# Kernel optimization log

Hardware: AMD Instinct MI355X
Metric: run time of the kernel (lower is better)

Reference implementation:

```python
import math
import jax, jax.numpy as jnp
import numpy as np

N_GAUSS = 1_000_000
EPS = 1e-8


def setup_inputs() -> dict:
    key = jax.random.key(0)
    k1, k2, k3 = jax.random.split(key, 3)
    init_extent = 50.0
    means = (jax.random.uniform(k1, (N_GAUSS, 3), dtype=jnp.float32) - 0.5) * 2.0 * init_extent
    log_scales = jnp.full((N_GAUSS, 3), math.log(0.05), dtype=jnp.float32)
    quats = jax.random.normal(k2, (N_GAUSS, 4), dtype=jnp.float32)
    sh_coeffs = jax.random.normal(k3, (N_GAUSS, 16, 3), dtype=jnp.float32) * 0.01
    opa_logit = math.log(0.1 / 0.9)  # inverse_sigmoid(init_opacity=0.1)
    opacity_camera = jnp.full((N_GAUSS, 1), opa_logit, dtype=jnp.float32)
    opacity_lidar = jnp.full((N_GAUSS, 1), opa_logit, dtype=jnp.float32)
    camera_to_world = jnp.eye(4, dtype=jnp.float32)
    lidar_to_world = jnp.eye(4, dtype=jnp.float32)
    intrinsics = jnp.array([[1000.0, 0.0, 800.0], [0.0, 1000.0, 450.0], [0.0, 0.0, 1.0]], dtype=jnp.float32)
    return dict(means=means, log_scales=log_scales, quats=quats, sh_coeffs=sh_coeffs,
                opacity_camera=opacity_camera, opacity_lidar=opacity_lidar,
                camera_to_world=camera_to_world, intrinsics=intrinsics,
                lidar_to_world=lidar_to_world,
                rgb_width=1600, rgb_height=900, lidar_width=1024, lidar_height=128,
                fov_min_deg=-25, fov_max_deg=3, near_plane=1, far_plane=100)


def _bilinear_scatter(u, v, w, vals, H, W, wrap_u):
    """Scatter vals [N,C] with weights w [N] at continuous pixel coords (u,v)
    using bilinear splatting. Returns [H, W, C+1] (weighted vals, weight sum)."""
    u0 = jnp.floor(u)
    v0 = jnp.floor(v)
    fu = u - u0
    fv = v - v0
    u0i = u0.astype(jnp.int32)
    v0i = v0.astype(jnp.int32)
    acc = jnp.zeros((H * W, vals.shape[-1] + 1), dtype=vals.dtype)
    corners = ((0, 0, (1.0 - fu) * (1.0 - fv)), (1, 0, fu * (1.0 - fv)),
               (0, 1, (1.0 - fu) * fv), (1, 1, fu * fv))
    for du, dv, cw in corners:
        ui = u0i + du
        vi = v0i + dv
        if wrap_u:
            ui = jnp.mod(ui, W)
            ok_u = jnp.ones_like(ui, dtype=bool)
        else:
            ok_u = (ui >= 0) & (ui < W)
        ok = ok_u & (vi >= 0) & (vi < H)
        ww = w * cw * ok.astype(w.dtype)
        idx = jnp.clip(vi, 0, H - 1) * W + jnp.clip(ui, 0, W - 1)
        payload = jnp.concatenate([vals * ww[:, None], ww[:, None]], axis=-1)
        acc = acc.at[idx].add(payload)
    return acc.reshape(H, W, -1)


def reference(means, log_scales, quats, sh_coeffs, opacity_camera, opacity_lidar,
              camera_to_world, intrinsics, lidar_to_world,
              rgb_width, rgb_height, lidar_width, lidar_height,
              fov_min_deg, fov_max_deg, near_plane, far_plane):
    H, W = int(rgb_height), int(rgb_width)
    HL, WL = int(lidar_height), int(lidar_width)
    near = float(near_plane)
    far = float(far_plane)

    # ---- camera (point-splat proxy of gsplat rasterization) ----
    w2c = jnp.linalg.inv(camera_to_world)
    pts_c = means @ w2c[:3, :3].T + w2c[:3, 3]  # [N,3] camera frame
    x, y, z = pts_c[:, 0], pts_c[:, 1], pts_c[:, 2]
    valid_c = (z > near) & (z < far)
    zs = jnp.where(valid_c, z, 1.0)
    u = intrinsics[0, 0] * x / zs + intrinsics[0, 2]
    v = intrinsics[1, 1] * y / zs + intrinsics[1, 2]
    opa_c = jax.nn.sigmoid(jnp.clip(opacity_camera[:, 0], -20.0, 20.0))
    colors = jax.nn.sigmoid(sh_coeffs[:, 0, :])  # DC band, as in render_rgb
    wc = opa_c * valid_c.astype(opa_c.dtype)
    vals_c = jnp.concatenate([colors, z[:, None]], axis=-1)  # [N,4] (rgb, depth)
    acc = _bilinear_scatter(u, v, wc, vals_c, H, W, wrap_u=False)
    wsum = acc[..., 4]
    alpha = jnp.clip(wsum, 0.0, 1.0)
    rgb = acc[..., :3] / (wsum[..., None] + EPS) * alpha[..., None]  # black background
    depth = acc[..., 3] / (wsum + EPS)

    # ---- LiDAR (custom spherical bilinear range-image splat, mean aggregation) ----
    w2l = jnp.linalg.inv(lidar_to_world)
    pts_l = means @ w2l[:3, :3].T + w2l[:3, 3]
    r = jnp.linalg.norm(pts_l, axis=-1)
    az = jnp.arctan2(pts_l[:, 1], pts_l[:, 0])
    el = jnp.arcsin(pts_l[:, 2] / jnp.maximum(r, 1e-6))
    fmin = math.radians(float(fov_min_deg))
    fmax = math.radians(float(fov_max_deg))
    uL = (az / (2.0 * jnp.pi) + 0.5) * WL          # azimuth wraps around
    vL = (fmax - el) / (fmax - fmin) * (HL - 1)    # elevation row
    valid_l = (r > near) & (r < far) & (el >= fmin) & (el <= fmax)
    opa_l = jax.nn.sigmoid(jnp.clip(opacity_lidar[:, 0], -20.0, 20.0))
    wl = opa_l * valid_l.astype(opa_l.dtype)
    acc_l = _bilinear_scatter(uL, vL, wl, r[:, None], HL, WL, wrap_u=True)
    lw = acc_l[..., 1]
    lidar_depth = acc_l[..., 0] / (lw + EPS)  # 'mean' depth aggregation
    lidar_alpha = jnp.clip(lw, 0.0, 1.0)

    return (rgb, depth, alpha, lidar_depth, lidar_alpha)
```

## Files before the change

kernel.cpp:

```cpp
#include <hip/hip_runtime.h>
#include <math.h>

#define EPSV 1e-8f
#define PI_D 3.14159265358979323846

__device__ void invert4x4(const float* m, float* out) {
    double a[4][8];
    for (int i = 0; i < 4; i++) {
        for (int j = 0; j < 4; j++) {
            a[i][j] = (double)m[i * 4 + j];
            a[i][j + 4] = (i == j) ? 1.0 : 0.0;
        }
    }
    for (int c = 0; c < 4; c++) {
        int p = c;
        double best = fabs(a[c][c]);
        for (int r = c + 1; r < 4; r++) {
            double v = fabs(a[r][c]);
            if (v > best) { best = v; p = r; }
        }
        if (p != c) {
            for (int j = 0; j < 8; j++) { double t = a[c][j]; a[c][j] = a[p][j]; a[p][j] = t; }
        }
        double piv = a[c][c];
        for (int j = 0; j < 8; j++) a[c][j] /= piv;
        for (int r = 0; r < 4; r++) {
            if (r == c) continue;
            double f = a[r][c];
            for (int j = 0; j < 8; j++) a[r][j] -= f * a[c][j];
        }
    }
    for (int i = 0; i < 4; i++)
        for (int j = 0; j < 4; j++)
            out[i * 4 + j] = (float)a[i][j + 4];
}

__global__ void prep_kernel(const float* __restrict__ c2w,
                            const float* __restrict__ l2w,
                            float* __restrict__ ws) {
    if (blockIdx.x == 0 && threadIdx.x == 0) {
        invert4x4(c2w, ws);
        invert4x4(l2w, ws + 16);
    }
}

__device__ __forceinline__ float sigmoid_clipped(float x) {
    x = fminf(fmaxf(x, -20.0f), 20.0f);
    return 1.0f / (1.0f + expf(-x));
}

__global__ __launch_bounds__(256) void scatter_kernel(
    const float* __restrict__ means,
    const float* __restrict__ sh,
    const float* __restrict__ opa_c,
    const float* __restrict__ opa_l,
    const float* __restrict__ intr,
    const float* __restrict__ ws,
    const int* __restrict__ p_W, const int* __restrict__ p_H,
    const int* __restrict__ p_WL, const int* __restrict__ p_HL,
    const int* __restrict__ p_fmin, const int* __restrict__ p_fmax,
    const int* __restrict__ p_near, const int* __restrict__ p_far,
    float* __restrict__ out, int N)
{
    #pragma clang fp contract(off)
    int i = blockIdx.x * blockDim.x + threadIdx.x;
    if (i >= N) return;

    const int W = *p_W, H = *p_H, WL = *p_WL, HL = *p_HL;
    const float nearp = (float)(*p_near);
    const float farp  = (float)(*p_far);
    const double dfmin = (double)(*p_fmin) * PI_D / 180.0;
    const double dfmax = (double)(*p_fmax) * PI_D / 180.0;
    const float ffmin  = (float)dfmin;
    const float ffmax  = (float)dfmax;
    const float denomL = (float)(dfmax - dfmin);
    const float twopi  = (float)(2.0 * PI_D);

    const long long HW = (long long)W * H;
    const long long LHW = (long long)WL * HL;
    const long long depthOff = 3 * HW;
    const long long alphaOff = 4 * HW;
    const long long ldOff    = 5 * HW;
    const long long laOff    = 5 * HW + LHW;

    const float mx = means[3 * i + 0];
    const float my = means[3 * i + 1];
    const float mz = means[3 * i + 2];

    {
        const float* w2c = ws;
        float x = w2c[0] * mx + w2c[1] * my + w2c[2]  * mz + w2c[3];
        float y = w2c[4] * mx + w2c[5] * my + w2c[6]  * mz + w2c[7];
        float z = w2c[8] * mx + w2c[9] * my + w2c[10] * mz + w2c[11];
        if (z > nearp && z < farp) {
            float u = intr[0] * x / z + intr[2];
            float v = intr[4] * y / z + intr[5];
            float wc = sigmoid_clipped(opa_c[i]);
            float c0 = 1.0f / (1.0f + expf(-sh[48 * i + 0]));
            float c1 = 1.0f / (1.0f + expf(-sh[48 * i + 1]));
            float c2 = 1.0f / (1.0f + expf(-sh[48 * i + 2]));

            float u0f = floorf(u), v0f = floorf(v);
            float fu = u - u0f, fv = v - v0f;
            int u0 = (int)u0f, v0 = (int)v0f;
            #pragma unroll
            for (int k = 0; k < 4; k++) {
                int du = k & 1, dv = k >> 1;
                int ui = u0 + du, vi = v0 + dv;
                if (ui >= 0 && ui < W && vi >= 0 && vi < H) {
                    float cw = (du ? fu : 1.0f - fu) * (dv ? fv : 1.0f - fv);
                    float ww = wc * cw;
                    long long idx = (long long)vi * W + ui;
                    atomicAdd(&out[idx * 3 + 0], c0 * ww);
                    atomicAdd(&out[idx * 3 + 1], c1 * ww);
                    atomicAdd(&out[idx * 3 + 2], c2 * ww);
                    atomicAdd(&out[depthOff + idx], z * ww);
                    atomicAdd(&out[alphaOff + idx], ww);
                }
            }
        }
    }

    {
        const float* w2l = ws + 16;
        float x = w2l[0] * mx + w2l[1] * my + w2l[2]  * mz + w2l[3];
        float y = w2l[4] * mx + w2l[5] * my + w2l[6]  * mz + w2l[7];
        float z = w2l[8] * mx + w2l[9] * my + w2l[10] * mz + w2l[11];
        float rr = ((x * x) + (y * y)) + (z * z);
        float r = sqrtf(rr);
        float q  = z / fmaxf(r, 1e-6f);
        float el = (float)asin((double)q);
        if (r > nearp && r < farp && el >= ffmin && el <= ffmax) {
            float az = (float)atan2((double)y, (double)x);
            float uL = (az / twopi + 0.5f) * (float)WL;
            float vL = (ffmax - el) / denomL * (float)(HL - 1);
            float wl = sigmoid_clipped(opa_l[i]);

            float u0f = floorf(uL), v0f = floorf(vL);
            float fu = uL - u0f, fv = vL - v0f;
            int u0 = (int)u0f, v0 = (int)v0f;
            #pragma unroll
            for (int k = 0; k < 4; k++) {
                int du = k & 1, dv = k >> 1;
                int ui = u0 + du, vi = v0 + dv;
                ui %= WL; if (ui < 0) ui += WL;
                if (vi >= 0 && vi < HL) {
                    float cw = (du ? fu : 1.0f - fu) * (dv ? fv : 1.0f - fv);
                    float ww = wl * cw;
                    long long idx = (long long)vi * WL + ui;
                    atomicAdd(&out[ldOff + idx], r * ww);
                    atomicAdd(&out[laOff + idx], ww);
                }
            }
        }
    }
}

__global__ __launch_bounds__(256) void finalize_kernel(
    float* __restrict__ out,
    const int* __restrict__ p_W, const int* __restrict__ p_H,
    const int* __restrict__ p_WL, const int* __restrict__ p_HL)
{
    const int W = *p_W, H = *p_H, WL = *p_WL, HL = *p_HL;
    const long long HW = (long long)W * H;
    const long long LHW = (long long)WL * HL;
    const long long depthOff = 3 * HW;
    const long long alphaOff = 4 * HW;
    const long long ldOff    = 5 * HW;
    const long long laOff    = 5 * HW + LHW;

    long long i = (long long)blockIdx.x * blockDim.x + threadIdx.x;
    if (i < HW) {
        float wsum = out[alphaOff + i];
        float a = fminf(fmaxf(wsum, 0.0f), 1.0f);
        float inv = 1.0f / (wsum + EPSV);
        float s = inv * a;
        out[3 * i + 0] *= s;
        out[3 * i + 1] *= s;
        out[3 * i + 2] *= s;
        out[depthOff + i] *= inv;
        out[alphaOff + i] = a;
    }
    if (i < LHW) {
        float wsum = out[laOff + i];
        out[ldOff + i] *= 1.0f / (wsum + EPSV);
        out[laOff + i] = fminf(fmaxf(wsum, 0.0f), 1.0f);
    }
}

extern "C" void kernel_launch(void* const* d_in, const int* in_sizes, int n_in,
                              void* d_out, int out_size, void* d_ws, size_t ws_size,
                              hipStream_t stream) {
    const float* means  = (const float*)d_in[0];
    const float* sh     = (const float*)d_in[3];
    const float* opa_c  = (const float*)d_in[4];
    const float* opa_l  = (const float*)d_in[5];
    const float* c2w    = (const float*)d_in[6];
    const float* intr   = (const float*)d_in[7];
    const float* l2w    = (const float*)d_in[8];
    const int* p_W    = (const int*)d_in[9];
    const int* p_H    = (const int*)d_in[10];
    const int* p_WL   = (const int*)d_in[11];
    const int* p_HL   = (const int*)d_in[12];
    const int* p_fmin = (const int*)d_in[13];
    const int* p_fmax = (const int*)d_in[14];
    const int* p_near = (const int*)d_in[15];
    const int* p_far  = (const int*)d_in[16];

    const int N = in_sizes[0] / 3;
    float* out = (float*)d_out;
    float* ws  = (float*)d_ws;

    hipMemsetAsync(d_out, 0, (size_t)out_size * sizeof(float), stream);

    prep_kernel<<<1, 64, 0, stream>>>(c2w, l2w, ws);

    scatter_kernel<<<(N + 255) / 256, 256, 0, stream>>>(
        means, sh, opa_c, opa_l, intr, ws,
        p_W, p_H, p_WL, p_HL, p_fmin, p_fmax, p_near, p_far,
        out, N);

    const long long HW = 1600LL * 900LL;
    finalize_kernel<<<(int)((HW + 255) / 256), 256, 0, stream>>>(
        out, p_W, p_H, p_WL, p_HL);
}
```

Measured before the change: 426.2 us.

## Process four Gaussians per thread and use closed-form 4x4 inverse

```diff
diff --git a/kernel.cpp b/kernel.cpp
--- a/kernel.cpp
+++ b/kernel.cpp
@@ -4,47 +4,58 @@
 #define EPSV 1e-8f
 #define PI_D 3.14159265358979323846
 
-__device__ void invert4x4(const float* m, float* out) {
-    double a[4][8];
-    for (int i = 0; i < 4; i++) {
-        for (int j = 0; j < 4; j++) {
-            a[i][j] = (double)m[i * 4 + j];
-            a[i][j + 4] = (i == j) ? 1.0 : 0.0;
-        }
-    }
-    for (int c = 0; c < 4; c++) {
-        int p = c;
-        double best = fabs(a[c][c]);
-        for (int r = c + 1; r < 4; r++) {
-            double v = fabs(a[r][c]);
-            if (v > best) { best = v; p = r; }
-        }
-        if (p != c) {
-            for (int j = 0; j < 8; j++) { double t = a[c][j]; a[c][j] = a[p][j]; a[p][j] = t; }
-        }
-        double piv = a[c][c];
-        for (int j = 0; j < 8; j++) a[c][j] /= piv;
-        for (int r = 0; r < 4; r++) {
-            if (r == c) continue;
-            double f = a[r][c];
-            for (int j = 0; j < 8; j++) a[r][j] -= f * a[c][j];
-        }
-    }
-    for (int i = 0; i < 4; i++)
-        for (int j = 0; j < 4; j++)
-            out[i * 4 + j] = (float)a[i][j + 4];
+__device__ __forceinline__ void invert4x4_reg(const float* __restrict__ m,
+                                              float* __restrict__ out) {
+    double a00=m[0], a01=m[1], a02=m[2], a03=m[3];
+    double a10=m[4], a11=m[5], a12=m[6], a13=m[7];
+    double a20=m[8], a21=m[9], a22=m[10],a23=m[11];
+    double a30=m[12],a31=m[13],a32=m[14],a33=m[15];
+
+    double b00 = a00*a11 - a01*a10;
+    double b01 = a00*a12 - a02*a10;
+    double b02 = a00*a13 - a03*a10;
+    double b03 = a01*a12 - a02*a11;
+    double b04 = a01*a13 - a03*a11;
+    double b05 = a02*a13 - a03*a12;
+    double b06 = a20*a31 - a21*a30;
+    double b07 = a20*a32 - a22*a30;
+    double b08 = a20*a33 - a23*a30;
+    double b09 = a21*a32 - a22*a31;
+    double b10 = a21*a33 - a23*a31;
+    double b11 = a22*a33 - a23*a32;
+
+    double det = b00*b11 - b01*b10 + b02*b09 + b03*b08 - b04*b07 + b05*b06;
+    double inv = 1.0 / det;
+
+    out[0]  = (float)(( a11*b11 - a12*b10 + a13*b09) * inv);
+    out[1]  = (float)((-a01*b11 + a02*b10 - a03*b09) * inv);
+    out[2]  = (float)(( a31*b05 - a32*b04 + a33*b03) * inv);
+    out[3]  = (float)((-a21*b05 + a22*b04 - a23*b03) * inv);
+    out[4]  = (float)((-a10*b11 + a12*b08 - a13*b07) * inv);
+    out[5]  = (float)(( a00*b11 - a02*b08 + a03*b07) * inv);
+    out[6]  = (float)((-a30*b05 + a32*b02 - a33*b01) * inv);
+    out[7]  = (float)(( a20*b05 - a22*b02 + a23*b01) * inv);
+    out[8]  = (float)(( a10*b10 - a11*b08 + a13*b06) * inv);
+    out[9]  = (float)((-a00*b10 + a01*b08 - a03*b06) * inv);
+    out[10] = (float)(( a30*b04 - a31*b02 + a33*b00) * inv);
+    out[11] = (float)((-a20*b04 + a21*b02 - a23*b00) * inv);
+    out[12] = (float)((-a10*b09 + a11*b07 - a12*b06) * inv);
+    out[13] = (float)(( a00*b09 - a01*b07 + a02*b06) * inv);
+    out[14] = (float)((-a30*b03 + a31*b01 - a32*b00) * inv);
+    out[15] = (float)(( a20*b03 - a21*b01 + a22*b00) * inv);
 }
 
 __global__ void prep_kernel(const float* __restrict__ c2w,
                             const float* __restrict__ l2w,
                             float* __restrict__ ws) {
     if (blockIdx.x == 0 && threadIdx.x == 0) {
-        invert4x4(c2w, ws);
-        invert4x4(l2w, ws + 16);
+        invert4x4_reg(c2w, ws);
+        invert4x4_reg(l2w, ws + 16);
     }
 }
 
 __device__ __forceinline__ float sigmoid_clipped(float x) {
+    #pragma clang fp contract(off)
     x = fminf(fmaxf(x, -20.0f), 20.0f);
     return 1.0f / (1.0f + expf(-x));
 }
@@ -63,8 +74,9 @@
     float* __restrict__ out, int N)
 {
     #pragma clang fp contract(off)
-    int i = blockIdx.x * blockDim.x + threadIdx.x;
-    if (i >= N) return;
+    const int T = (N + 3) >> 2;
+    const int t = blockIdx.x * blockDim.x + threadIdx.x;
+    if (t >= T) return;
 
     const int W = *p_W, H = *p_H, WL = *p_WL, HL = *p_HL;
     const float nearp = (float)(*p_near);
@@ -83,73 +95,94 @@
     const long long ldOff    = 5 * HW;
     const long long laOff    = 5 * HW + LHW;
 
-    const float mx = means[3 * i + 0];
-    const float my = means[3 * i + 1];
-    const float mz = means[3 * i + 2];
-
-    {
-        const float* w2c = ws;
-        float x = w2c[0] * mx + w2c[1] * my + w2c[2]  * mz + w2c[3];
-        float y = w2c[4] * mx + w2c[5] * my + w2c[6]  * mz + w2c[7];
-        float z = w2c[8] * mx + w2c[9] * my + w2c[10] * mz + w2c[11];
-        if (z > nearp && z < farp) {
-            float u = intr[0] * x / z + intr[2];
-            float v = intr[4] * y / z + intr[5];
-            float wc = sigmoid_clipped(opa_c[i]);
-            float c0 = 1.0f / (1.0f + expf(-sh[48 * i + 0]));
-            float c1 = 1.0f / (1.0f + expf(-sh[48 * i + 1]));
-            float c2 = 1.0f / (1.0f + expf(-sh[48 * i + 2]));
-
-            float u0f = floorf(u), v0f = floorf(v);
-            float fu = u - u0f, fv = v - v0f;
-            int u0 = (int)u0f, v0 = (int)v0f;
-            #pragma unroll
-            for (int k = 0; k < 4; k++) {
-                int du = k & 1, dv = k >> 1;
-                int ui = u0 + du, vi = v0 + dv;
-                if (ui >= 0 && ui < W && vi >= 0 && vi < H) {
-                    float cw = (du ? fu : 1.0f - fu) * (dv ? fv : 1.0f - fv);
-                    float ww = wc * cw;
-                    long long idx = (long long)vi * W + ui;
-                    atomicAdd(&out[idx * 3 + 0], c0 * ww);
-                    atomicAdd(&out[idx * 3 + 1], c1 * ww);
-                    atomicAdd(&out[idx * 3 + 2], c2 * ww);
-                    atomicAdd(&out[depthOff + idx], z * ww);
-                    atomicAdd(&out[alphaOff + idx], ww);
+    const float fx = intr[0], cx = intr[2], fy = intr[4], cy = intr[5];
+    const float* w2c = ws;
+    const float* w2l = ws + 16;
+
+    float mx[4], my[4], mz[4], oc[4], ol[4];
+    int   gi[4];
+    bool  gv[4];
+    #pragma unroll
+    for (int k = 0; k < 4; k++) {
+        int i = t + k * T;
+        gv[k] = (i < N);
+        int ii = gv[k] ? i : 0;
+        gi[k] = ii;
+        mx[k] = means[3 * ii + 0];
+        my[k] = means[3 * ii + 1];
+        mz[k] = means[3 * ii + 2];
+        oc[k] = opa_c[ii];
+        ol[k] = opa_l[ii];
+    }
+
+    #pragma unroll
+    for (int k = 0; k < 4; k++) {
+        if (!gv[k]) continue;
+        const float px = mx[k], py = my[k], pz = mz[k];
+
+        {
+            float x = w2c[0] * px + w2c[1] * py + w2c[2]  * pz + w2c[3];
+            float y = w2c[4] * px + w2c[5] * py + w2c[6]  * pz + w2c[7];
+            float z = w2c[8] * px + w2c[9] * py + w2c[10] * pz + w2c[11];
+            if (z > nearp && z < farp) {
+                float u = fx * x / z + cx;
+                float v = fy * y / z + cy;
+                float wc = sigmoid_clipped(oc[k]);
+                const float* shp = sh + 48LL * gi[k];
+                float c0 = 1.0f / (1.0f + expf(-shp[0]));
+                float c1 = 1.0f / (1.0f + expf(-shp[1]));
+                float c2 = 1.0f / (1.0f + expf(-shp[2]));
+
+                float u0f = floorf(u), v0f = floorf(v);
+                float fu = u - u0f, fv = v - v0f;
+                int u0 = (int)u0f, v0 = (int)v0f;
+                #pragma unroll
+                for (int c = 0; c < 4; c++) {
+                    int du = c & 1, dv = c >> 1;
+                    int ui = u0 + du, vi = v0 + dv;
+                    if (ui >= 0 && ui < W && vi >= 0 && vi < H) {
+                        float cw = (du ? fu : 1.0f - fu) * (dv ? fv : 1.0f - fv);
+                        float ww = wc * cw;
+                        long long idx = (long long)vi * W + ui;
+                        atomicAdd(&out[idx * 3 + 0], c0 * ww);
+                        atomicAdd(&out[idx * 3 + 1], c1 * ww);
+                        atomicAdd(&out[idx * 3 + 2], c2 * ww);
+                        atomicAdd(&out[depthOff + idx], z * ww);
+                        atomicAdd(&out[alphaOff + idx], ww);
+                    }
                 }
             }
         }
-    }
-
-    {
-        const float* w2l = ws + 16;
-        float x = w2l[0] * mx + w2l[1] * my + w2l[2]  * mz + w2l[3];
-        float y = w2l[4] * mx + w2l[5] * my + w2l[6]  * mz + w2l[7];
-        float z = w2l[8] * mx + w2l[9] * my + w2l[10] * mz + w2l[11];
-        float rr = ((x * x) + (y * y)) + (z * z);
-        float r = sqrtf(rr);
-        float q  = z / fmaxf(r, 1e-6f);
-        float el = (float)asin((double)q);
-        if (r > nearp && r < farp && el >= ffmin && el <= ffmax) {
-            float az = (float)atan2((double)y, (double)x);
-            float uL = (az / twopi + 0.5f) * (float)WL;
-            float vL = (ffmax - el) / denomL * (float)(HL - 1);
-            float wl = sigmoid_clipped(opa_l[i]);
-
-            float u0f = floorf(uL), v0f = floorf(vL);
-            float fu = uL - u0f, fv = vL - v0f;
-            int u0 = (int)u0f, v0 = (int)v0f;
-            #pragma unroll
-            for (int k = 0; k < 4; k++) {
-                int du = k & 1, dv = k >> 1;
-                int ui = u0 + du, vi = v0 + dv;
-                ui %= WL; if (ui < 0) ui += WL;
-                if (vi >= 0 && vi < HL) {
-                    float cw = (du ? fu : 1.0f - fu) * (dv ? fv : 1.0f - fv);
-                    float ww = wl * cw;
-                    long long idx = (long long)vi * WL + ui;
-                    atomicAdd(&out[ldOff + idx], r * ww);
-                    atomicAdd(&out[laOff + idx], ww);
+
+        {
+            float x = w2l[0] * px + w2l[1] * py + w2l[2]  * pz + w2l[3];
+            float y = w2l[4] * px + w2l[5] * py + w2l[6]  * pz + w2l[7];
+            float z = w2l[8] * px + w2l[9] * py + w2l[10] * pz + w2l[11];
+            float rr = ((x * x) + (y * y)) + (z * z);
+            float r = sqrtf(rr);
+            float q  = z / fmaxf(r, 1e-6f);
+            float el = (float)asin((double)q);
+            if (r > nearp && r < farp && el >= ffmin && el <= ffmax) {
+                float az = (float)atan2((double)y, (double)x);
+                float uL = (az / twopi + 0.5f) * (float)WL;
+                float vL = (ffmax - el) / denomL * (float)(HL - 1);
+                float wl = sigmoid_clipped(ol[k]);
+
+                float u0f = floorf(uL), v0f = floorf(vL);
+                float fu = uL - u0f, fv = vL - v0f;
+                int u0 = (int)u0f, v0 = (int)v0f;
+                #pragma unroll
+                for (int c = 0; c < 4; c++) {
+                    int du = c & 1, dv = c >> 1;
+                    int ui = u0 + du, vi = v0 + dv;
+                    ui %= WL; if (ui < 0) ui += WL;
+                    if (vi >= 0 && vi < HL) {
+                        float cw = (du ? fu : 1.0f - fu) * (dv ? fv : 1.0f - fv);
+                        float ww = wl * cw;
+                        long long idx = (long long)vi * WL + ui;
+                        atomicAdd(&out[ldOff + idx], r * ww);
+                        atomicAdd(&out[laOff + idx], ww);
+                    }
                 }
             }
         }
@@ -215,7 +248,8 @@
 
     prep_kernel<<<1, 64, 0, stream>>>(c2w, l2w, ws);
 
-    scatter_kernel<<<(N + 255) / 256, 256, 0, stream>>>(
+    const int T = (N + 3) / 4;
+    scatter_kernel<<<(T + 255) / 256, 256, 0, stream>>>(
         means, sh, opa_c, opa_l, intr, ws,
         p_W, p_H, p_WL, p_HL, p_fmin, p_fmax, p_near, p_far,
         out, N);
```

Measured after the change: 423.9 us. Within noise of the previous version (-0.5%).
